# Performance work log

Hardware: AMD Instinct MI355X
Metric: run time of the kernel (lower is better)

Reference implementation:

```python
import jax, jax.numpy as jnp
import numpy as np

B, N, F = 512, 2048, 64
T = 4            # number of atom types
H1, H2 = 64, 32  # hidden widths; final layer outputs 1 (per-atom energy)


def setup_inputs() -> dict:
    key = jax.random.key(0)
    ks = jax.random.split(key, 8)
    x = jax.random.normal(ks[0], (B, N, F), dtype=jnp.float32)
    atomic_numbers = jax.random.randint(ks[1], (N,), 0, T)
    s = 0.05
    # Per-type MLP parameters, stacked over the type axis (torch Linear layout: [out, in]).
    w0 = jax.random.normal(ks[2], (T, H1, F), dtype=jnp.float32) * s
    b0 = jax.random.normal(ks[3], (T, H1), dtype=jnp.float32) * s
    w1 = jax.random.normal(ks[4], (T, H2, H1), dtype=jnp.float32) * s
    b1 = jax.random.normal(ks[5], (T, H2), dtype=jnp.float32) * s
    w2 = jax.random.normal(ks[6], (T, 1, H2), dtype=jnp.float32) * s
    b2 = jax.random.normal(ks[7], (T, 1), dtype=jnp.float32) * s
    return {"x": x, "atomic_numbers": atomic_numbers,
            "w0": w0, "b0": b0, "w1": w1, "b1": b1, "w2": w2, "b2": b2}


def reference(x, atomic_numbers, w0, b0, w1, b1, w2, b2):
    # Behler-Parrinello: route each atom through the MLP of its atom type,
    # then sum per-atom energies over atoms.  The torch version gathers atoms
    # by type, runs each type's MLP, and scatters back; here we evaluate all
    # T type-MLPs batched over the type axis and select with a one-hot mask
    # (identical math, jit-friendly, no data-dependent shapes).
    onehot = jax.nn.one_hot(atomic_numbers, w0.shape[0], dtype=x.dtype)  # [N, T]
    h = jax.nn.silu(jnp.einsum('bnf,thf->tbnh', x, w0) + b0[:, None, None, :])   # [T,B,N,H1]
    h = jax.nn.silu(jnp.einsum('tbnh,tgh->tbng', h, w1) + b1[:, None, None, :])  # [T,B,N,H2]
    e = jnp.einsum('tbng,tog->tbno', h, w2) + b2[:, None, None, :]               # [T,B,N,1]
    e = e[..., 0]                                                                # [T,B,N]
    per_atom = jnp.einsum('tbn,nt->bn', e, onehot)  # select the matching type per atom
    return per_atom.sum(axis=-1)                    # [B]
```

## Files before the change

### kernel.cpp

```cpp
#include <hip/hip_runtime.h>
#include <hip/hip_bf16.h>


#define B_ 512
#define N_ 2048
#define F_ 64
#define T_ 4
#define H1_ 64
#define H2_ 32

#define BT 16
#define WAVES 4
#define NCHUNK 128

typedef __attribute__((ext_vector_type(8))) short bf16x8;
typedef __attribute__((ext_vector_type(4))) short bf16x4;
typedef __attribute__((ext_vector_type(4))) float f32x4;

__device__ inline float silu_f(float v) {
    return v * __builtin_amdgcn_rcpf(1.0f + __expf(-v));
}

__device__ inline bf16x8 pack8(float4 a, float4 b) {
    union { __hip_bfloat162 h[4]; bf16x8 v; } u;
    u.h[0] = __float22bfloat162_rn({a.x, a.y});
    u.h[1] = __float22bfloat162_rn({a.z, a.w});
    u.h[2] = __float22bfloat162_rn({b.x, b.y});
    u.h[3] = __float22bfloat162_rn({b.z, b.w});
    return u.v;
}

__device__ inline bf16x4 pack4(float a, float b, float c, float d) {
    union { __hip_bfloat162 h[2]; bf16x4 v; } u;
    u.h[0] = __float22bfloat162_rn({a, b});
    u.h[1] = __float22bfloat162_rn({c, d});
    return u.v;
}

__device__ inline float bf_at(bf16x4 v, int r) {
    union { bf16x4 v; __hip_bfloat16 h[4]; } u; u.v = v;
    return __bfloat162float(u.h[r]);
}

__global__ __launch_bounds__(256, 3) void bpnn_kernel(
    const float* __restrict__ x, const int* __restrict__ an,
    const float* __restrict__ w0, const float* __restrict__ b0,
    const float* __restrict__ w1, const float* __restrict__ b1,
    const float* __restrict__ w2, const float* __restrict__ b2,
    float* __restrict__ out)
{
    __shared__ __align__(16) __hip_bfloat16 trb[WAVES][BT][68];
    __shared__ int sidx[NCHUNK];
    __shared__ int cnt[T_], offs[T_], pos[T_];
    __shared__ float red[BT];

    const int tid  = threadIdx.x;
    const int wave = tid >> 6;
    const int lane = tid & 63;
    const int lr   = lane & 15;
    const int q    = lane >> 4;
    const int b0i  = blockIdx.y * BT;
    const int n0   = blockIdx.x * NCHUNK;
    const int t    = wave;

    const float* w0t = w0 + t * (H1_ * F_);
    const float* w1t = w1 + t * (H2_ * H1_);
    bf16x8 aw0[4][2], aw1[2][2];
#pragma unroll
    for (int nt = 0; nt < 4; ++nt)
#pragma unroll
        for (int kh = 0; kh < 2; ++kh) {
            const float4* p = reinterpret_cast<const float4*>(
                w0t + (nt * 16 + lr) * F_ + kh * 32 + q * 8);
            aw0[nt][kh] = pack8(p[0], p[1]);
        }
#pragma unroll
    for (int mt = 0; mt < 2; ++mt)
#pragma unroll
        for (int kh = 0; kh < 2; ++kh) {
            const float4* p = reinterpret_cast<const float4*>(
                w1t + (mt * 16 + lr) * H1_ + kh * 32 + q * 8);
            aw1[mt][kh] = pack8(p[0], p[1]);
        }
    bf16x4 b0f[4], b1f[2], w2f[2];
#pragma unroll
    for (int nt = 0; nt < 4; ++nt) {
        float4 v = *reinterpret_cast<const float4*>(b0 + t * H1_ + nt * 16 + q * 4);
        b0f[nt] = pack4(v.x, v.y, v.z, v.w);
    }
#pragma unroll
    for (int mt = 0; mt < 2; ++mt) {
        float4 v = *reinterpret_cast<const float4*>(b1 + t * H2_ + mt * 16 + q * 4);
        b1f[mt] = pack4(v.x, v.y, v.z, v.w);
        float4 u = *reinterpret_cast<const float4*>(w2 + t * H2_ + mt * 16 + q * 4);
        w2f[mt] = pack4(u.x, u.y, u.z, u.w);
    }
    const float b2t = b2[t];

    if (tid < T_)  cnt[tid] = 0;
    if (tid < BT)  red[tid] = 0.0f;
    __syncthreads();
    int myt = 0;
    if (tid < NCHUNK) { myt = an[n0 + tid]; atomicAdd(&cnt[myt], 1); }
    __syncthreads();
    if (tid == 0) {
        int o = 0;
        for (int k = 0; k < T_; ++k) { offs[k] = o; pos[k] = o; o += cnt[k]; }
    }
    __syncthreads();
    if (tid < NCHUNK) { int p = atomicAdd(&pos[myt], 1); sidx[p] = tid; }
    __syncthreads();

    const int beg = offs[t];
    const int num = __builtin_amdgcn_readfirstlane(cnt[t]);

    const float* xb_ = x + (size_t)(b0i + lr) * (N_ * F_) + (size_t)n0 * F_ + q * 8;
    __hip_bfloat16* trbw = &trb[wave][lr][0];

    float esum = 0.f;

    if (num > 0) {
        int nl = sidx[beg];
        const float4* p0 = reinterpret_cast<const float4*>(xb_ + nl * F_);
        float4 pa = p0[0], pb = p0[1], pc = p0[8], pd = p0[9];

        for (int it = 0; it < num; ++it) {
            bf16x8 xf0 = pack8(pa, pb);
            bf16x8 xf1 = pack8(pc, pd);
            {
                int ii = (it + 1 < num) ? (it + 1) : it;
                int nn = sidx[beg + ii];
                const float4* pn = reinterpret_cast<const float4*>(xb_ + nn * F_);
                pa = pn[0]; pb = pn[1]; pc = pn[8]; pd = pn[9];
            }

            f32x4 acc[4] = {{0,0,0,0},{0,0,0,0},{0,0,0,0},{0,0,0,0}};
#pragma unroll
            for (int nt = 0; nt < 4; ++nt) {
                acc[nt] = __builtin_amdgcn_mfma_f32_16x16x32_bf16(aw0[nt][0], xf0, acc[nt], 0, 0, 0);
                acc[nt] = __builtin_amdgcn_mfma_f32_16x16x32_bf16(aw0[nt][1], xf1, acc[nt], 0, 0, 0);
            }
#pragma unroll
            for (int nt = 0; nt < 4; ++nt) {
                float v0 = silu_f(acc[nt][0] + bf_at(b0f[nt], 0));
                float v1 = silu_f(acc[nt][1] + bf_at(b0f[nt], 1));
                float v2 = silu_f(acc[nt][2] + bf_at(b0f[nt], 2));
                float v3 = silu_f(acc[nt][3] + bf_at(b0f[nt], 3));
                *reinterpret_cast<bf16x4*>(trbw + nt * 16 + q * 4) = pack4(v0, v1, v2, v3);
            }
            __builtin_amdgcn_wave_barrier();

            bf16x8 hb0 = *reinterpret_cast<const bf16x8*>(trbw + q * 8);
            bf16x8 hb1 = *reinterpret_cast<const bf16x8*>(trbw + 32 + q * 8);
            __builtin_amdgcn_wave_barrier();

            f32x4 accB[2] = {{0,0,0,0},{0,0,0,0}};
#pragma unroll
            for (int mt = 0; mt < 2; ++mt) {
                accB[mt] = __builtin_amdgcn_mfma_f32_16x16x32_bf16(aw1[mt][0], hb0, accB[mt], 0, 0, 0);
                accB[mt] = __builtin_amdgcn_mfma_f32_16x16x32_bf16(aw1[mt][1], hb1, accB[mt], 0, 0, 0);
            }
#pragma unroll
            for (int mt = 0; mt < 2; ++mt) {
#pragma unroll
                for (int r = 0; r < 4; ++r) {
                    float v = silu_f(accB[mt][r] + bf_at(b1f[mt], r));
                    esum += v * bf_at(w2f[mt], r);
                }
            }
        }
    }

    esum += __shfl_xor(esum, 16);
    esum += __shfl_xor(esum, 32);
    if (q == 0) atomicAdd(&red[lr], esum + (float)num * b2t);
    __syncthreads();
    if (tid < BT) atomicAdd(&out[b0i + tid], red[tid]);
}

extern "C" void kernel_launch(void* const* d_in, const int* in_sizes, int n_in,
                              void* d_out, int out_size, void* d_ws, size_t ws_size,
                              hipStream_t stream) {
    const float* x  = (const float*)d_in[0];
    const int*   an = (const int*)d_in[1];
    const float* w0 = (const float*)d_in[2];
    const float* b0 = (const float*)d_in[3];
    const float* w1 = (const float*)d_in[4];
    const float* b1 = (const float*)d_in[5];
    const float* w2 = (const float*)d_in[6];
    const float* b2 = (const float*)d_in[7];
    float* out = (float*)d_out;

    hipMemsetAsync(out, 0, B_ * sizeof(float), stream);
    dim3 grid(N_ / NCHUNK, B_ / BT);
    bpnn_kernel<<<grid, 256, 0, stream>>>(x, an, w0, b0, w1, b1, w2, b2, out);
}
```

Baseline: 383.0 us.

## Chain layer-2 MFMA directly from layer-1 accumulators, skip LDS transpose

Uses 16x16x16 bf16 MFMA for the second layer so the first layer's output accumulator fragments can be fed straight in as B operands. This removes the per-iteration LDS write/read transpose and the wave barriers around it. Biases are now preloaded into the accumulators in fp32 instead of being added as bf16 after the MFMA, and w2 is kept in fp32. Launch bounds drop to 2 blocks per CU to allow more registers, which costs occupancy. The second layer now issues 8 smaller MFMAs instead of 4 larger ones.

Measured after the change: 384.4 us. About the same (+0.4%).

```diff
diff --git a/kernel.cpp b/kernel.cpp
--- a/kernel.cpp
+++ b/kernel.cpp
@@ -16,6 +16,16 @@
 typedef __attribute__((ext_vector_type(8))) short bf16x8;
 typedef __attribute__((ext_vector_type(4))) short bf16x4;
 typedef __attribute__((ext_vector_type(4))) float f32x4;
+
+#if __has_builtin(__builtin_amdgcn_mfma_f32_16x16x16_bf16)
+#define MFMA16(A, Bv, C) __builtin_amdgcn_mfma_f32_16x16x16_bf16((A), (Bv), (C), 0, 0, 0)
+#define HAVE_MFMA16 1
+#elif __has_builtin(__builtin_amdgcn_mfma_f32_16x16x16bf16_1k)
+#define MFMA16(A, Bv, C) __builtin_amdgcn_mfma_f32_16x16x16bf16_1k((A), (Bv), (C), 0, 0, 0)
+#define HAVE_MFMA16 1
+#else
+#define HAVE_MFMA16 0
+#endif
 
 __device__ inline float silu_f(float v) {
     return v * __builtin_amdgcn_rcpf(1.0f + __expf(-v));
@@ -37,19 +47,16 @@
     return u.v;
 }
 
-__device__ inline float bf_at(bf16x4 v, int r) {
-    union { bf16x4 v; __hip_bfloat16 h[4]; } u; u.v = v;
-    return __bfloat162float(u.h[r]);
-}
-
-__global__ __launch_bounds__(256, 3) void bpnn_kernel(
+__global__ __launch_bounds__(256, 2) void bpnn_kernel(
     const float* __restrict__ x, const int* __restrict__ an,
     const float* __restrict__ w0, const float* __restrict__ b0,
     const float* __restrict__ w1, const float* __restrict__ b1,
     const float* __restrict__ w2, const float* __restrict__ b2,
     float* __restrict__ out)
 {
+#if !HAVE_MFMA16
     __shared__ __align__(16) __hip_bfloat16 trb[WAVES][BT][68];
+#endif
     __shared__ int sidx[NCHUNK];
     __shared__ int cnt[T_], offs[T_], pos[T_];
     __shared__ float red[BT];
@@ -65,7 +72,7 @@
 
     const float* w0t = w0 + t * (H1_ * F_);
     const float* w1t = w1 + t * (H2_ * H1_);
-    bf16x8 aw0[4][2], aw1[2][2];
+    bf16x8 aw0[4][2];
 #pragma unroll
     for (int nt = 0; nt < 4; ++nt)
 #pragma unroll
@@ -74,6 +81,18 @@
                 w0t + (nt * 16 + lr) * F_ + kh * 32 + q * 8);
             aw0[nt][kh] = pack8(p[0], p[1]);
         }
+#if HAVE_MFMA16
+    bf16x4 aw1[2][4];
+#pragma unroll
+    for (int mt = 0; mt < 2; ++mt)
+#pragma unroll
+        for (int nt = 0; nt < 4; ++nt) {
+            float4 v = *reinterpret_cast<const float4*>(
+                w1t + (mt * 16 + lr) * H1_ + nt * 16 + q * 4);
+            aw1[mt][nt] = pack4(v.x, v.y, v.z, v.w);
+        }
+#else
+    bf16x8 aw1[2][2];
 #pragma unroll
     for (int mt = 0; mt < 2; ++mt)
 #pragma unroll
@@ -82,18 +101,15 @@
                 w1t + (mt * 16 + lr) * H1_ + kh * 32 + q * 8);
             aw1[mt][kh] = pack8(p[0], p[1]);
         }
-    bf16x4 b0f[4], b1f[2], w2f[2];
-#pragma unroll
-    for (int nt = 0; nt < 4; ++nt) {
-        float4 v = *reinterpret_cast<const float4*>(b0 + t * H1_ + nt * 16 + q * 4);
-        b0f[nt] = pack4(v.x, v.y, v.z, v.w);
-    }
+#endif
+    f32x4 b0v[4], b1v[2], w2v[2];
+#pragma unroll
+    for (int nt = 0; nt < 4; ++nt)
+        b0v[nt] = *reinterpret_cast<const f32x4*>(b0 + t * H1_ + nt * 16 + q * 4);
 #pragma unroll
     for (int mt = 0; mt < 2; ++mt) {
-        float4 v = *reinterpret_cast<const float4*>(b1 + t * H2_ + mt * 16 + q * 4);
-        b1f[mt] = pack4(v.x, v.y, v.z, v.w);
-        float4 u = *reinterpret_cast<const float4*>(w2 + t * H2_ + mt * 16 + q * 4);
-        w2f[mt] = pack4(u.x, u.y, u.z, u.w);
+        b1v[mt] = *reinterpret_cast<const f32x4*>(b1 + t * H2_ + mt * 16 + q * 4);
+        w2v[mt] = *reinterpret_cast<const f32x4*>(w2 + t * H2_ + mt * 16 + q * 4);
     }
     const float b2t = b2[t];
 
@@ -115,7 +131,9 @@
     const int num = __builtin_amdgcn_readfirstlane(cnt[t]);
 
     const float* xb_ = x + (size_t)(b0i + lr) * (N_ * F_) + (size_t)n0 * F_ + q * 8;
+#if !HAVE_MFMA16
     __hip_bfloat16* trbw = &trb[wave][lr][0];
+#endif
 
     float esum = 0.f;
 
@@ -134,40 +152,44 @@
                 pa = pn[0]; pb = pn[1]; pc = pn[8]; pd = pn[9];
             }
 
-            f32x4 acc[4] = {{0,0,0,0},{0,0,0,0},{0,0,0,0},{0,0,0,0}};
+            f32x4 acc[4] = {b0v[0], b0v[1], b0v[2], b0v[3]};
 #pragma unroll
             for (int nt = 0; nt < 4; ++nt) {
                 acc[nt] = __builtin_amdgcn_mfma_f32_16x16x32_bf16(aw0[nt][0], xf0, acc[nt], 0, 0, 0);
                 acc[nt] = __builtin_amdgcn_mfma_f32_16x16x32_bf16(aw0[nt][1], xf1, acc[nt], 0, 0, 0);
             }
-#pragma unroll
-            for (int nt = 0; nt < 4; ++nt) {
-                float v0 = silu_f(acc[nt][0] + bf_at(b0f[nt], 0));
-                float v1 = silu_f(acc[nt][1] + bf_at(b0f[nt], 1));
-                float v2 = silu_f(acc[nt][2] + bf_at(b0f[nt], 2));
-                float v3 = silu_f(acc[nt][3] + bf_at(b0f[nt], 3));
-                *reinterpret_cast<bf16x4*>(trbw + nt * 16 + q * 4) = pack4(v0, v1, v2, v3);
-            }
+            bf16x4 hb[4];
+#pragma unroll
+            for (int nt = 0; nt < 4; ++nt)
+                hb[nt] = pack4(silu_f(acc[nt][0]), silu_f(acc[nt][1]),
+                               silu_f(acc[nt][2]), silu_f(acc[nt][3]));
+
+            f32x4 accB[2] = {b1v[0], b1v[1]};
+#if HAVE_MFMA16
+#pragma unroll
+            for (int mt = 0; mt < 2; ++mt)
+#pragma unroll
+                for (int nt = 0; nt < 4; ++nt)
+                    accB[mt] = MFMA16(aw1[mt][nt], hb[nt], accB[mt]);
+#else
+#pragma unroll
+            for (int nt = 0; nt < 4; ++nt)
+                *reinterpret_cast<bf16x4*>(trbw + nt * 16 + q * 4) = hb[nt];
             __builtin_amdgcn_wave_barrier();
-
             bf16x8 hb0 = *reinterpret_cast<const bf16x8*>(trbw + q * 8);
             bf16x8 hb1 = *reinterpret_cast<const bf16x8*>(trbw + 32 + q * 8);
             __builtin_amdgcn_wave_barrier();
-
-            f32x4 accB[2] = {{0,0,0,0},{0,0,0,0}};
 #pragma unroll
             for (int mt = 0; mt < 2; ++mt) {
                 accB[mt] = __builtin_amdgcn_mfma_f32_16x16x32_bf16(aw1[mt][0], hb0, accB[mt], 0, 0, 0);
                 accB[mt] = __builtin_amdgcn_mfma_f32_16x16x32_bf16(aw1[mt][1], hb1, accB[mt], 0, 0, 0);
             }
-#pragma unroll
-            for (int mt = 0; mt < 2; ++mt) {
-#pragma unroll
-                for (int r = 0; r < 4; ++r) {
-                    float v = silu_f(accB[mt][r] + bf_at(b1f[mt], r));
-                    esum += v * bf_at(w2f[mt], r);
-                }
-            }
+#endif
+#pragma unroll
+            for (int mt = 0; mt < 2; ++mt)
+#pragma unroll
+                for (int r = 0; r < 4; ++r)
+                    esum += silu_f(accB[mt][r]) * w2v[mt][r];
         }
     }
 
```
